# Kernel optimization log

Hardware: AMD Instinct MI355X
Metric: run time of the kernel (lower is better)

## Reference

```python
import jax, jax.numpy as jnp
import numpy as np
import math

B, S, E, H = 8, 1024, 512, 8
EPS = 1e-5

def _ln(x, g, b):
    mu = jnp.mean(x, axis=-1, keepdims=True)
    var = jnp.mean(jnp.square(x - mu), axis=-1, keepdims=True)
    return (x - mu) * jax.lax.rsqrt(var + EPS) * g + b

def setup_inputs() -> dict:
    key = jax.random.key(0)
    ks = iter(jax.random.split(key, 40))
    def w(shape, scale=0.02):
        return jax.random.normal(next(ks), shape, dtype=jnp.float32) * scale
    inp = {
        'x': jax.random.normal(next(ks), (B, S, E), dtype=jnp.float32),
        'cond': jax.random.normal(next(ks), (B, 1, E), dtype=jnp.float32),
        # AdaLN modulation linears (stored as (in,out))
        'g1w': w((E, E)), 'g1b': jnp.zeros((E,), jnp.float32),
        'be1w': w((E, E)), 'be1b': jnp.zeros((E,), jnp.float32),
        'a1w': w((E, E)), 'a1b': jnp.zeros((E,), jnp.float32),
        'g2w': w((E, E)), 'g2b': jnp.zeros((E,), jnp.float32),
        'be2w': w((E, E)), 'be2b': jnp.zeros((E,), jnp.float32),
        'a2w': w((E, E)), 'a2b': jnp.zeros((E,), jnp.float32),
        # LayerNorm affine
        'ln1g': jnp.ones((E,), jnp.float32), 'ln1b': jnp.zeros((E,), jnp.float32),
        'ln2g': jnp.ones((E,), jnp.float32), 'ln2b': jnp.zeros((E,), jnp.float32),
        # attention projections: each head has width E -> out dim H*E
        'wq': w((E, H * E)), 'bq': jnp.zeros((H * E,), jnp.float32),
        'wk': w((E, H * E)), 'bk': jnp.zeros((H * E,), jnp.float32),
        'wv': w((E, H * E)), 'bv': jnp.zeros((H * E,), jnp.float32),
        'lvw': w((H * E, E)), 'lvb': jnp.zeros((E,), jnp.float32),
        # FFN
        'f1w': w((E, 4 * E)), 'f1b': jnp.zeros((4 * E,), jnp.float32),
        'f2w': w((4 * E, E)), 'f2b': jnp.zeros((E,), jnp.float32),
    }
    return inp

def reference(x, cond, g1w, g1b, be1w, be1b, a1w, a1b, g2w, g2b, be2w, be2b, a2w, a2b,
              ln1g, ln1b, ln2g, ln2b, wq, bq, wk, bk, wv, bv, lvw, lvb, f1w, f1b, f2w, f2b):
    # AdaLN modulation signals, each (B,1,E)
    gamma1 = cond @ g1w + g1b
    beta1 = cond @ be1w + be1b
    alpha1 = cond @ a1w + a1b
    gamma2 = cond @ g2w + g2b
    beta2 = cond @ be2w + be2b
    alpha2 = cond @ a2w + a2b

    y = _ln(x, ln1g, ln1b) * (1.0 + gamma1) + beta1
    q = (y @ wq + bq).reshape(B, S, H, E).transpose(0, 2, 1, 3)  # (B,H,S,E)
    k = (y @ wk + bk).reshape(B, S, H, E).transpose(0, 2, 1, 3)
    v = (y @ wv + bv).reshape(B, S, H, E).transpose(0, 2, 1, 3)
    # NOTE: original scales by sqrt(q.size(2)) == sqrt(seq_len), not head_dim
    scale = 1.0 / math.sqrt(S)
    attn = jax.nn.softmax(jnp.einsum('bhse,bhte->bhst', q, k) * scale, axis=-1)
    o = jnp.einsum('bhst,bhte->bhse', attn, v)  # (B,H,S,E)
    o = o.transpose(0, 2, 1, 3).reshape(B, S, H * E)
    y = x + (o @ lvw + lvb) * alpha1

    z = _ln(y, ln2g, ln2b) * (1.0 + gamma2) + beta2
    z = (jax.nn.relu(z @ f1w + f1b) @ f2w + f2b) * alpha2
    return y + z
```

## Files before the change

### kernel.cpp

```cpp
#include <hip/hip_runtime.h>
#include <hip/hip_bf16.h>

typedef __bf16 bf16_t;
typedef bf16_t bf16x8 __attribute__((ext_vector_type(8)));
typedef bf16_t bf16x4 __attribute__((ext_vector_type(4)));
typedef float f32x4 __attribute__((ext_vector_type(4)));

typedef const __attribute__((address_space(1))) void GV;
typedef __attribute__((address_space(3))) void LV;

__device__ __forceinline__ void gload_lds16(const bf16_t* gsrc, bf16_t* ldst) {
    __builtin_amdgcn_global_load_lds((GV*)gsrc, (LV*)ldst, 16, 0, 0);
}

__global__ __launch_bounds__(256) void prep_kernel(
    const float* __restrict__ wq, const float* __restrict__ wk, const float* __restrict__ wv,
    const float* __restrict__ lvw, const float* __restrict__ f1w, const float* __restrict__ f2w,
    bf16_t* __restrict__ wqT, bf16_t* __restrict__ lvwT,
    bf16_t* __restrict__ f1wT, bf16_t* __restrict__ f2wT,
    const float* __restrict__ cond,
    const float* __restrict__ mw0, const float* __restrict__ mw1, const float* __restrict__ mw2,
    const float* __restrict__ mw3, const float* __restrict__ mw4, const float* __restrict__ mw5,
    const float* __restrict__ mc0, const float* __restrict__ mc1, const float* __restrict__ mc2,
    const float* __restrict__ mc3, const float* __restrict__ mc4, const float* __restrict__ mc5,
    float* __restrict__ mod)
{
    __shared__ float sbuf[32 * 33];
    const int bid = blockIdx.x;
    if (bid < 10240) {
        float (*tile)[33] = (float(*)[33])sbuf;
        const float* in; bf16_t* out; int N, nx, K, local;
        if (bid < 6144) {
            const int sec = bid >> 11;
            local = bid & 2047;
            in = (sec == 0) ? wq : ((sec == 1) ? wk : wv);
            out = wqT + (long long)sec * 2097152;
            K = 512; N = 4096; nx = 128;
        } else if (bid < 8192) {
            local = bid - 6144; in = lvw; out = lvwT; K = 4096; N = 512; nx = 16;
        } else if (bid < 9216) {
            local = bid - 8192; in = f1w; out = f1wT; K = 512; N = 2048; nx = 64;
        } else {
            local = bid - 9216; in = f2w; out = f2wT; K = 2048; N = 512; nx = 16;
        }
        const int n0 = (local % nx) * 32, k0 = (local / nx) * 32;
        const int tx = threadIdx.x & 31, ty = threadIdx.x >> 5;
#pragma unroll
        for (int i = 0; i < 32; i += 8)
            tile[ty + i][tx] = in[(long long)(k0 + ty + i) * N + n0 + tx];
        __syncthreads();
#pragma unroll
        for (int i = 0; i < 32; i += 8)
            out[(long long)(n0 + ty + i) * K + k0 + tx] = (bf16_t)tile[tx][ty + i];
    } else {
        float* cs = sbuf;
        const int lb = bid - 10240;
        const int sig = lb >> 3, b = lb & 7;
        const float* w; const float* bi;
        switch (sig) {
            case 0: w = mw0; bi = mc0; break;
            case 1: w = mw1; bi = mc1; break;
            case 2: w = mw2; bi = mc2; break;
            case 3: w = mw3; bi = mc3; break;
            case 4: w = mw4; bi = mc4; break;
            default: w = mw5; bi = mc5; break;
        }
        for (int i = threadIdx.x; i < 512; i += 256) cs[i] = cond[b * 512 + i];
        __syncthreads();
        for (int n = threadIdx.x; n < 512; n += 256) {
            float s0 = 0.f, s1 = 0.f, s2 = 0.f, s3 = 0.f;
            for (int i = 0; i < 512; i += 4) {
                s0 = fmaf(cs[i], w[(long long)i * 512 + n], s0);
                s1 = fmaf(cs[i + 1], w[(long long)(i + 1) * 512 + n], s1);
                s2 = fmaf(cs[i + 2], w[(long long)(i + 2) * 512 + n], s2);
                s3 = fmaf(cs[i + 3], w[(long long)(i + 3) * 512 + n], s3);
            }
            mod[(long long)(sig * 8 + b) * 512 + n] = bi[n] + (s0 + s1) + (s2 + s3);
        }
    }
}

__global__ __launch_bounds__(128) void ln_mod_kernel(
    const float* __restrict__ x, const float* __restrict__ g, const float* __restrict__ be,
    const float* __restrict__ gamma, const float* __restrict__ beta, bf16_t* __restrict__ out)
{
    const int row = blockIdx.x;
    const int b = row >> 10;
    const int t = threadIdx.x;
    const float4 v = reinterpret_cast<const float4*>(x + (long long)row * 512)[t];
    float s = v.x + v.y + v.z + v.w;
    float ss = v.x * v.x + v.y * v.y + v.z * v.z + v.w * v.w;
    for (int o = 32; o; o >>= 1) { s += __shfl_xor(s, o); ss += __shfl_xor(ss, o); }
    __shared__ float red[4];
    if ((t & 63) == 0) { red[t >> 6] = s; red[2 + (t >> 6)] = ss; }
    __syncthreads();
    s = red[0] + red[1]; ss = red[2] + red[3];
    const float mu = s * (1.f / 512.f);
    const float rstd = rsqrtf(ss * (1.f / 512.f) - mu * mu + 1e-5f);
    const float4 gv = reinterpret_cast<const float4*>(g)[t];
    const float4 bv = reinterpret_cast<const float4*>(be)[t];
    const float4 ga = reinterpret_cast<const float4*>(gamma + b * 512)[t];
    const float4 bb = reinterpret_cast<const float4*>(beta + b * 512)[t];
    bf16x4 ov;
    ov[0] = (bf16_t)(((v.x - mu) * rstd * gv.x + bv.x) * (1.f + ga.x) + bb.x);
    ov[1] = (bf16_t)(((v.y - mu) * rstd * gv.y + bv.y) * (1.f + ga.y) + bb.y);
    ov[2] = (bf16_t)(((v.z - mu) * rstd * gv.z + bv.z) * (1.f + ga.z) + bb.z);
    ov[3] = (bf16_t)(((v.w - mu) * rstd * gv.w + bv.w) * (1.f + ga.w) + bb.w);
    reinterpret_cast<bf16x4*>(out + (long long)row * 512)[t] = ov;
}

template <int EPI>
__global__ __launch_bounds__(256) void gemm128_kernel(
    const bf16_t* __restrict__ A, const bf16_t* __restrict__ B,
    const float* __restrict__ bias, void* Cout,
    int M, int N, int K, int lda, int ldb, int ldc)
{
    const int nbx = gridDim.x;
    const int lin = blockIdx.y * nbx + blockIdx.x;
    const int cpx = (nbx * gridDim.y) >> 3;
    const int swz = (lin & 7) * cpx + (lin >> 3);
    const int m0 = (swz / nbx) * 128, n0 = (swz % nbx) * 128;
    const int tid = threadIdx.x, lane = tid & 63, wid = tid >> 6;
    const int wr = wid >> 1, wc = wid & 1;

    __shared__ bf16_t As[16384];
    __shared__ bf16_t Bs[16384];

    f32x4 acc[4][4];
#pragma unroll
    for (int m = 0; m < 4; ++m)
#pragma unroll
        for (int n = 0; n < 4; ++n) acc[m][n] = (f32x4){0.f, 0.f, 0.f, 0.f};

    const int r8 = lane >> 3;
    const int lc = (lane & 7) ^ r8;
    long long aOff[4], bOff[4];
#pragma unroll
    for (int i = 0; i < 4; ++i) {
        const int row = i * 32 + wid * 8 + r8;
        aOff[i] = (long long)(m0 + row) * lda + lc * 8;
        bOff[i] = (long long)(n0 + row) * ldb + lc * 8;
    }

    const int frow = lane & 15, lg = lane >> 4;
    const int p0 = lg ^ (frow & 7);

#pragma unroll
    for (int i = 0; i < 4; ++i) gload_lds16(A + aOff[i], As + i * 2048 + wid * 512);
#pragma unroll
    for (int i = 0; i < 4; ++i) gload_lds16(B + bOff[i], Bs + i * 2048 + wid * 512);

    for (int kt = 0; kt < K; kt += 64) {
        const int cur = (kt >> 6) & 1;
        __syncthreads();
        if (kt + 64 < K) {
            const int nxt = (cur ^ 1) * 8192;
#pragma unroll
            for (int i = 0; i < 4; ++i) gload_lds16(A + aOff[i] + kt + 64, As + nxt + i * 2048 + wid * 512);
#pragma unroll
            for (int i = 0; i < 4; ++i) gload_lds16(B + bOff[i] + kt + 64, Bs + nxt + i * 2048 + wid * 512);
        }
        const bf16_t* Ab = As + cur * 8192;
        const bf16_t* Bb = Bs + cur * 8192;
        __builtin_amdgcn_s_setprio(1);
#pragma unroll
        for (int kk = 0; kk < 2; ++kk) {
            const int pc = p0 ^ (kk << 2);
            bf16x8 af[4], bfv[4];
#pragma unroll
            for (int m = 0; m < 4; ++m)
                af[m] = *reinterpret_cast<const bf16x8*>(Ab + (wr * 64 + m * 16 + frow) * 64 + pc * 8);
#pragma unroll
            for (int n = 0; n < 4; ++n)
                bfv[n] = *reinterpret_cast<const bf16x8*>(Bb + (wc * 64 + n * 16 + frow) * 64 + pc * 8);
#pragma unroll
            for (int m = 0; m < 4; ++m)
#pragma unroll
                for (int n = 0; n < 4; ++n)
                    acc[m][n] = __builtin_amdgcn_mfma_f32_16x16x32_bf16(af[m], bfv[n], acc[m][n], 0, 0, 0);
        }
        __builtin_amdgcn_s_setprio(0);
    }

#pragma unroll
    for (int m = 0; m < 4; ++m) {
        const int gm = m0 + wr * 64 + m * 16 + ((lane >> 4) << 2);
#pragma unroll
        for (int n = 0; n < 4; ++n) {
            const int gn = n0 + wc * 64 + n * 16 + (lane & 15);
            const float bb = bias ? bias[gn] : 0.f;
#pragma unroll
            for (int j = 0; j < 4; ++j) {
                const float v = acc[m][n][j] + bb;
                const int gmj = gm + j;
                if (EPI == 0) {
                    ((bf16_t*)Cout)[(long long)gmj * ldc + gn] = (bf16_t)v;
                } else {
                    ((bf16_t*)Cout)[(long long)gmj * ldc + gn] = (bf16_t)fmaxf(v, 0.f);
                }
            }
        }
    }
}

__global__ __launch_bounds__(256) void gemmqkv_kernel(
    const bf16_t* __restrict__ A, const bf16_t* __restrict__ B,
    const float* __restrict__ bq, const float* __restrict__ bk, const float* __restrict__ bv,
    bf16_t* __restrict__ qkv, bf16_t* __restrict__ vtb)
{
    const int lin = blockIdx.y * 96 + blockIdx.x;
    const int swz = (lin & 7) * 768 + (lin >> 3);
    const int m0 = (swz / 96) * 128, n0 = (swz % 96) * 128;
    const int sec = n0 >> 12;
    const float* bias = (sec == 0) ? bq : ((sec == 1) ? bk : bv);
    const int tid = threadIdx.x, lane = tid & 63, wid = tid >> 6;
    const int wr = wid >> 1, wc = wid & 1;

    __shared__ bf16_t As[16384];
    __shared__ bf16_t Bs[16384];

    f32x4 acc[4][4];
#pragma unroll
    for (int m = 0; m < 4; ++m)
#pragma unroll
        for (int n = 0; n < 4; ++n) acc[m][n] = (f32x4){0.f, 0.f, 0.f, 0.f};

    const int r8 = lane >> 3;
    const int lc = (lane & 7) ^ r8;
    long long aOff[4], bOff[4];
#pragma unroll
    for (int i = 0; i < 4; ++i) {
        const int row = i * 32 + wid * 8 + r8;
        aOff[i] = (long long)(m0 + row) * 512 + lc * 8;
        bOff[i] = (long long)(n0 + row) * 512 + lc * 8;
    }

    const int frow = lane & 15, lg = lane >> 4;
    const int p0 = lg ^ (frow & 7);

#pragma unroll
    for (int i = 0; i < 4; ++i) gload_lds16(A + aOff[i], As + i * 2048 + wid * 512);
#pragma unroll
    for (int i = 0; i < 4; ++i) gload_lds16(B + bOff[i], Bs + i * 2048 + wid * 512);

    for (int kt = 0; kt < 512; kt += 64) {
        const int cur = (kt >> 6) & 1;
        __syncthreads();
        if (kt + 64 < 512) {
            const int nxt = (cur ^ 1) * 8192;
#pragma unroll
            for (int i = 0; i < 4; ++i) gload_lds16(A + aOff[i] + kt + 64, As + nxt + i * 2048 + wid * 512);
#pragma unroll
            for (int i = 0; i < 4; ++i) gload_lds16(B + bOff[i] + kt + 64, Bs + nxt + i * 2048 + wid * 512);
        }
        const bf16_t* Ab = As + cur * 8192;
        const bf16_t* Bb = Bs + cur * 8192;
        __builtin_amdgcn_s_setprio(1);
#pragma unroll
        for (int kk = 0; kk < 2; ++kk) {
            const int pc = p0 ^ (kk << 2);
            bf16x8 af[4], bfv[4];
#pragma unroll
            for (int m = 0; m < 4; ++m)
                af[m] = *reinterpret_cast<const bf16x8*>(Ab + (wr * 64 + m * 16 + frow) * 64 + pc * 8);
#pragma unroll
            for (int n = 0; n < 4; ++n)
                bfv[n] = *reinterpret_cast<const bf16x8*>(Bb + (wc * 64 + n * 16 + frow) * 64 + pc * 8);
#pragma unroll
            for (int m = 0; m < 4; ++m)
#pragma unroll
                for (int n = 0; n < 4; ++n)
                    acc[m][n] = __builtin_amdgcn_mfma_f32_16x16x32_bf16(af[m], bfv[n], acc[m][n], 0, 0, 0);
        }
        __builtin_amdgcn_s_setprio(0);
    }

#pragma unroll
    for (int m = 0; m < 4; ++m) {
        const int gm = m0 + wr * 64 + m * 16 + ((lane >> 4) << 2);
#pragma unroll
        for (int n = 0; n < 4; ++n) {
            const int gn = n0 + wc * 64 + n * 16 + (lane & 15);
            const int gnl = gn & 4095;
            const float bb = bias[gnl];
#pragma unroll
            for (int j = 0; j < 4; ++j) {
                const float v = acc[m][n][j] + bb;
                const int gmj = gm + j;
                if (sec < 2) {
                    qkv[(long long)sec * 33554432 + (long long)gmj * 4096 + gnl] = (bf16_t)v;
                } else {
                    const long long ci =
                        (long long)(((gmj >> 10) * 8 + (gnl >> 9)) * 512 + (gnl & 511)) * 1024 + (gmj & 1023);
                    vtb[ci] = (bf16_t)v;
                }
            }
        }
    }
}

__global__ __launch_bounds__(256) void gemm64_kernel(
    const bf16_t* __restrict__ A, const bf16_t* __restrict__ B,
    const float* __restrict__ bias, float* __restrict__ Cout,
    const float* __restrict__ resid, const float* __restrict__ alpha,
    int M, int N, int K, int lda, int ldb)
{
    const int nbx = gridDim.x;
    const int lin = blockIdx.y * nbx + blockIdx.x;
    const int cpx = (nbx * gridDim.y) >> 3;
    const int swz = (lin & 7) * cpx + (lin >> 3);
    const int m0 = (swz / nbx) * 64, n0 = (swz % nbx) * 128;
    const int tid = threadIdx.x, lane = tid & 63, wid = tid >> 6;
    const int wr = wid >> 1, wc = wid & 1;

    __shared__ bf16_t As[8192];
    __shared__ bf16_t Bs[16384];

    f32x4 acc[2][4];
#pragma unroll
    for (int m = 0; m < 2; ++m)
#pragma unroll
        for (int n = 0; n < 4; ++n) acc[m][n] = (f32x4){0.f, 0.f, 0.f, 0.f};

    const int r8 = lane >> 3;
    const int lc = (lane & 7) ^ r8;
    long long aOff[2], bOff[4];
#pragma unroll
    for (int i = 0; i < 2; ++i)
        aOff[i] = (long long)(m0 + i * 32 + wid * 8 + r8) * lda + lc * 8;
#pragma unroll
    for (int i = 0; i < 4; ++i)
        bOff[i] = (long long)(n0 + i * 32 + wid * 8 + r8) * ldb + lc * 8;

    const int frow = lane & 15, lg = lane >> 4;
    const int p0 = lg ^ (frow & 7);

#pragma unroll
    for (int i = 0; i < 2; ++i) gload_lds16(A + aOff[i], As + i * 2048 + wid * 512);
#pragma unroll
    for (int i = 0; i < 4; ++i) gload_lds16(B + bOff[i], Bs + i * 2048 + wid * 512);

    for (int kt = 0; kt < K; kt += 64) {
        const int cur = (kt >> 6) & 1;
        __syncthreads();
        if (kt + 64 < K) {
#pragma unroll
            for (int i = 0; i < 2; ++i)
                gload_lds16(A + aOff[i] + kt + 64, As + (cur ^ 1) * 4096 + i * 2048 + wid * 512);
#pragma unroll
            for (int i = 0; i < 4; ++i)
                gload_lds16(B + bOff[i] + kt + 64, Bs + (cur ^ 1) * 8192 + i * 2048 + wid * 512);
        }
        const bf16_t* Ab = As + cur * 4096;
        const bf16_t* Bb = Bs + cur * 8192;
        __builtin_amdgcn_s_setprio(1);
#pragma unroll
        for (int kk = 0; kk < 2; ++kk) {
            const int pc = p0 ^ (kk << 2);
            bf16x8 af[2], bfv[4];
#pragma unroll
            for (int m = 0; m < 2; ++m)
                af[m] = *reinterpret_cast<const bf16x8*>(Ab + (wr * 32 + m * 16 + frow) * 64 + pc * 8);
#pragma unroll
            for (int n = 0; n < 4; ++n)
                bfv[n] = *reinterpret_cast<const bf16x8*>(Bb + (wc * 64 + n * 16 + frow) * 64 + pc * 8);
#pragma unroll
            for (int m = 0; m < 2; ++m)
#pragma unroll
                for (int n = 0; n < 4; ++n)
                    acc[m][n] = __builtin_amdgcn_mfma_f32_16x16x32_bf16(af[m], bfv[n], acc[m][n], 0, 0, 0);
        }
        __builtin_amdgcn_s_setprio(0);
    }

#pragma unroll
    for (int m = 0; m < 2; ++m) {
        const int gm = m0 + wr * 32 + m * 16 + ((lane >> 4) << 2);
#pragma unroll
        for (int n = 0; n < 4; ++n) {
            const int gn = n0 + wc * 64 + n * 16 + (lane & 15);
            const float bb = bias[gn];
#pragma unroll
            for (int j = 0; j < 4; ++j) {
                const int gmj = gm + j;
                const long long ci = (long long)gmj * 512 + gn;
                Cout[ci] = resid[ci] + (acc[m][n][j] + bb) * alpha[(gmj >> 10) * 512 + gn];
            }
        }
    }
}

#define FA_LDS 69632
#define SCL 0.04508422132207354f
__global__ __launch_bounds__(256, 2) void flash_kernel(
    bf16_t* __restrict__ qb, const bf16_t* __restrict__ kb, const bf16_t* __restrict__ vtb)
{
    extern __shared__ char smem[];
    bf16_t* Ks = (bf16_t*)smem;
    bf16_t* Vs = (bf16_t*)(smem + 32768);
    char* PB = smem + 65536;
    float* pmaxB = (float*)(smem + 67584);
    float* psumB = (float*)(smem + 68608);

    const int bid = blockIdx.x;
    const int xcd = bid & 7, idx = bid >> 3;
    const int qt = idx & 31, bhl = idx >> 5;
    const int bh = xcd * 8 + bhl;
    const int b = bh >> 3, h = bh & 7;
    const int q0 = qt * 32;
    const int tid = threadIdx.x, lane = tid & 63, wid = tid >> 6;
    const int laneq = lane & 15, lx = lane & 7, lg = lane >> 4;
    const int wk = wid >> 1, wq = wid & 1;
    const int we = wid;

#pragma unroll
    for (int r = 0; r < 8; ++r) {
        const int row = r * 4 + wid;
        gload_lds16(kb + ((long long)(b * 1024 + row) * 8 + h) * 512 + ((lane ^ (row & 7)) << 3),
                    Ks + row * 512);
    }
    const int qi = wq * 16 + laneq;
    bf16x8 qfrag[16];
    {
        const bf16_t* qrow = qb + ((long long)(b * 1024 + q0 + qi) * 8 + h) * 512 + lg * 8;
#pragma unroll
        for (int ks = 0; ks < 16; ++ks) qfrag[ks] = *reinterpret_cast<const bf16x8*>(qrow + ks * 32);
    }
    f32x4 accA[8], accB[8];
#pragma unroll
    for (int e = 0; e < 8; ++e) { accA[e] = (f32x4){0.f,0.f,0.f,0.f}; accB[e] = (f32x4){0.f,0.f,0.f,0.f}; }
    float mS = 0.f, mPA = 0.f, mPB = 0.f, lA = 0.f, lB = 0.f;
    const int rA = wk * 16 + laneq;
    const int qA = laneq, qB = laneq + 16;
    __syncthreads();

    for (int t = 0; t < 32; ++t) {
#pragma unroll
        for (int r = 0; r < 8; ++r) {
            const int e0 = (r * 4 + wid) * 16;
            const int e = e0 + (lane >> 2);
            gload_lds16(vtb + ((long long)bh * 512 + e) * 1024 + t * 32
                            + (((lane & 3) ^ ((e >> 1) & 3)) << 3),
                        Vs + e0 * 32);
        }
        f32x4 s0 = (f32x4){0.f, 0.f, 0.f, 0.f};
        const char* KsB = (const char*)Ks;
        __builtin_amdgcn_s_setprio(1);
#pragma unroll
        for (int ks = 0; ks < 16; ++ks) {
            const int co = (((ks * 4 + lg) ^ lx) << 4);
            bf16x8 a0 = *(const bf16x8*)(KsB + rA * 1024 + co);
            s0 = __builtin_amdgcn_mfma_f32_16x16x32_bf16(a0, qfrag[ks], s0, 0, 0, 0);
        }
        __builtin_amdgcn_s_setprio(0);
        float f[4], pe[4];
#pragma unroll
        for (int j = 0; j < 4; ++j) f[j] = s0[j] * SCL;
        float mloc = fmaxf(fmaxf(f[0], f[1]), fmaxf(f[2], f[3]));
        mloc = fmaxf(mloc, __shfl_xor(mloc, 16));
        mloc = fmaxf(mloc, __shfl_xor(mloc, 32));
        float sl = 0.f;
#pragma unroll
        for (int j = 0; j < 4; ++j) { pe[j] = exp2f(f[j] - mS); sl += pe[j]; }
        sl += __shfl_xor(sl, 16);
        sl += __shfl_xor(sl, 32);
        if (lane < 16) {
            const int si = (t & 1) * 64 + (wq * 16 + lane) * 2 + wk;
            pmaxB[si] = mloc;
            psumB[si] = sl;
        }
        {
            bf16x4 p;
#pragma unroll
            for (int j = 0; j < 4; ++j) p[j] = (bf16_t)pe[j];
            const int g = wk * 4 + lg;
            *(bf16x4*)(PB + qi * 64 + ((((g >> 1) ^ ((qi >> 1) & 3))) << 4) + ((g & 1) << 3)) = p;
        }
        __syncthreads();

        if (t < 31) {
#pragma unroll
            for (int r = 0; r < 8; ++r) {
                const int row = r * 4 + wid;
                gload_lds16(kb + ((long long)(b * 1024 + t * 32 + 32 + row) * 8 + h) * 512
                                + ((lane ^ (row & 7)) << 3),
                            Ks + row * 512);
            }
        }
        const char* VB = (const char*)Vs;
        bf16x8 pA = *(const bf16x8*)(PB + qA * 64 + ((lg ^ ((qA >> 1) & 3)) << 4));
        bf16x8 pBv = *(const bf16x8*)(PB + qB * 64 + ((lg ^ ((qB >> 1) & 3)) << 4));
        __builtin_amdgcn_s_setprio(1);
#pragma unroll
        for (int ef = 0; ef < 8; ++ef) {
            const int re = we * 128 + ef * 16 + laneq;
            bf16x8 av = *(const bf16x8*)(VB + re * 64 + ((lg ^ ((re >> 1) & 3)) << 4));
            accA[ef] = __builtin_amdgcn_mfma_f32_16x16x32_bf16(av, pA, accA[ef], 0, 0, 0);
            accB[ef] = __builtin_amdgcn_mfma_f32_16x16x32_bf16(av, pBv, accB[ef], 0, 0, 0);
        }
        __builtin_amdgcn_s_setprio(0);
        {
            const float* pmax_t = pmaxB + (t & 1) * 64;
            const float* psum_t = psumB + (t & 1) * 64;
            const float2 pmA = *(const float2*)&pmax_t[qA * 2];
            const float2 pmB = *(const float2*)&pmax_t[qB * 2];
            const float2 psA = *(const float2*)&psum_t[qA * 2];
            const float2 psB = *(const float2*)&psum_t[qB * 2];
            mS = fmaxf(mS, wq ? fmaxf(pmB.x, pmB.y) : fmaxf(pmA.x, pmA.y));
            lA += psA.x + psA.y;
            lB += psB.x + psB.y;
            const float mnA = fmaxf(mPA, fmaxf(pmA.x, pmA.y));
            const float mnB = fmaxf(mPB, fmaxf(pmB.x, pmB.y));
            if (__ballot((mnA > mPA) || (mnB > mPB))) {
                const float rsA = exp2f(mPA - mnA), rsB = exp2f(mPB - mnB);
                lA *= rsA; lB *= rsB;
#pragma unroll
                for (int e = 0; e < 8; ++e) {
#pragma unroll
                    for (int j = 0; j < 4; ++j) { accA[e][j] *= rsA; accB[e][j] *= rsB; }
                }
            }
            mPA = mnA; mPB = mnB;
        }
        __syncthreads();
    }

    const float iA = 1.f / lA, iB = 1.f / lB;
#pragma unroll
    for (int ef = 0; ef < 8; ++ef) {
        const int e0 = we * 128 + ef * 16 + lg * 4;
        bf16x4 oA, oB;
#pragma unroll
        for (int j = 0; j < 4; ++j) { oA[j] = (bf16_t)(accA[ef][j] * iA); oB[j] = (bf16_t)(accB[ef][j] * iB); }
        *(bf16x4*)(qb + ((long long)(b * 1024 + q0 + qA) * 8 + h) * 512 + e0) = oA;
        *(bf16x4*)(qb + ((long long)(b * 1024 + q0 + qB) * 8 + h) * 512 + e0) = oB;
    }
}

extern "C" void kernel_launch(void* const* d_in, const int* in_sizes, int n_in,
                              void* d_out, int out_size, void* d_ws, size_t ws_size,
                              hipStream_t stream)
{
    const float* x    = (const float*)d_in[0];
    const float* cond = (const float*)d_in[1];
    const float* g1w  = (const float*)d_in[2];  const float* g1b  = (const float*)d_in[3];
    const float* be1w = (const float*)d_in[4];  const float* be1b = (const float*)d_in[5];
    const float* a1w  = (const float*)d_in[6];  const float* a1b  = (const float*)d_in[7];
    const float* g2w  = (const float*)d_in[8];  const float* g2b  = (const float*)d_in[9];
    const float* be2w = (const float*)d_in[10]; const float* be2b = (const float*)d_in[11];
    const float* a2w  = (const float*)d_in[12]; const float* a2b  = (const float*)d_in[13];
    const float* ln1g = (const float*)d_in[14]; const float* ln1b = (const float*)d_in[15];
    const float* ln2g = (const float*)d_in[16]; const float* ln2b = (const float*)d_in[17];
    const float* wq   = (const float*)d_in[18]; const float* bq   = (const float*)d_in[19];
    const float* wk   = (const float*)d_in[20]; const float* bk   = (const float*)d_in[21];
    const float* wv   = (const float*)d_in[22]; const float* bv   = (const float*)d_in[23];
    const float* lvw  = (const float*)d_in[24]; const float* lvb  = (const float*)d_in[25];
    const float* f1w  = (const float*)d_in[26]; const float* f1b  = (const float*)d_in[27];
    const float* f2w  = (const float*)d_in[28]; const float* f2b  = (const float*)d_in[29];
    (void)in_sizes; (void)n_in; (void)out_size; (void)ws_size;

    char* w8 = (char*)d_ws;
    float*  mod  = (float*)(w8);
    bf16_t* wqT  = (bf16_t*)(w8 + 98304);
    bf16_t* lvwT = (bf16_t*)(w8 + 98304 + 3 * 4194304);
    bf16_t* f1wT = (bf16_t*)(w8 + 98304 + 4 * 4194304);
    bf16_t* f2wT = (bf16_t*)(w8 + 98304 + 4 * 4194304 + 2097152);
    bf16_t* ybf  = (bf16_t*)(w8 + 98304 + 4 * 4194304 + 2 * 2097152);
    bf16_t* qb   = (bf16_t*)(w8 + 98304 + 4 * 4194304 + 2 * 2097152 + 8388608);
    bf16_t* kb   = qb + 33554432;
    bf16_t* vtb  = kb + 33554432;

    (void)hipFuncSetAttribute((const void*)flash_kernel,
                              hipFuncAttributeMaxDynamicSharedMemorySize, FA_LDS);

    const dim3 blk(256);
    prep_kernel<<<10288, blk, 0, stream>>>(wq, wk, wv, lvw, f1w, f2w,
                                           wqT, lvwT, f1wT, f2wT,
                                           cond, g1w, be1w, a1w, g2w, be2w, a2w,
                                           g1b, be1b, a1b, g2b, be2b, a2b, mod);
    ln_mod_kernel<<<8192, 128, 0, stream>>>(x, ln1g, ln1b, mod, mod + 4096, ybf);
    gemmqkv_kernel<<<dim3(96, 64), blk, 0, stream>>>(ybf, wqT, bq, bk, bv, qb, vtb);
    flash_kernel<<<2048, 256, FA_LDS, stream>>>(qb, kb, vtb);
    gemm64_kernel<<<dim3(4, 128), blk, 0, stream>>>(qb, lvwT, lvb, (float*)d_out, x, mod + 8192,
        8192, 512, 4096, 4096, 4096);
    ln_mod_kernel<<<8192, 128, 0, stream>>>((const float*)d_out, ln2g, ln2b,
                                            mod + 12288, mod + 16384, ybf);
    gemm128_kernel<1><<<dim3(16, 64), blk, 0, stream>>>(ybf, f1wT, f1b, qb,
        8192, 2048, 512, 512, 512, 2048);
    gemm64_kernel<<<dim3(4, 128), blk, 0, stream>>>(qb, f2wT, f2b, (float*)d_out,
        (const float*)d_out, mod + 20480,
        8192, 512, 2048, 2048, 2048);
}
```

Baseline: 673.9 us.

## Enlarge QKV GEMM tile to 256x128, drop double buffering, split flash QK accumulators

The QKV projection GEMM now uses 256x128 block tiles, so each wave computes a 128x64 output with 8x4 MFMA accumulators. The grid is halved to match, and B-operand reuse per block goes up. The LDS double-buffered prefetch is replaced by a single buffer that loads and then syncs twice per k-step, which removes the overlap of loads with compute. In the flash kernel, the QK^T dot product now rotates across four independent accumulators to break the serial MFMA dependency chain, summing them at the end at the cost of extra registers.

```diff
diff --git a/kernel.cpp b/kernel.cpp
--- a/kernel.cpp
+++ b/kernel.cpp
@@ -209,75 +209,64 @@
     bf16_t* __restrict__ qkv, bf16_t* __restrict__ vtb)
 {
     const int lin = blockIdx.y * 96 + blockIdx.x;
-    const int swz = (lin & 7) * 768 + (lin >> 3);
-    const int m0 = (swz / 96) * 128, n0 = (swz % 96) * 128;
+    const int swz = (lin & 7) * 384 + (lin >> 3);
+    const int m0 = (swz / 96) * 256, n0 = (swz % 96) * 128;
     const int sec = n0 >> 12;
     const float* bias = (sec == 0) ? bq : ((sec == 1) ? bk : bv);
     const int tid = threadIdx.x, lane = tid & 63, wid = tid >> 6;
     const int wr = wid >> 1, wc = wid & 1;
 
     __shared__ bf16_t As[16384];
-    __shared__ bf16_t Bs[16384];
-
-    f32x4 acc[4][4];
-#pragma unroll
-    for (int m = 0; m < 4; ++m)
+    __shared__ bf16_t Bs[8192];
+
+    f32x4 acc[8][4];
+#pragma unroll
+    for (int m = 0; m < 8; ++m)
 #pragma unroll
         for (int n = 0; n < 4; ++n) acc[m][n] = (f32x4){0.f, 0.f, 0.f, 0.f};
 
     const int r8 = lane >> 3;
     const int lc = (lane & 7) ^ r8;
-    long long aOff[4], bOff[4];
-#pragma unroll
-    for (int i = 0; i < 4; ++i) {
-        const int row = i * 32 + wid * 8 + r8;
-        aOff[i] = (long long)(m0 + row) * 512 + lc * 8;
-        bOff[i] = (long long)(n0 + row) * 512 + lc * 8;
-    }
+    long long aOff[8], bOff[4];
+#pragma unroll
+    for (int i = 0; i < 8; ++i)
+        aOff[i] = (long long)(m0 + i * 32 + wid * 8 + r8) * 512 + lc * 8;
+#pragma unroll
+    for (int i = 0; i < 4; ++i)
+        bOff[i] = (long long)(n0 + i * 32 + wid * 8 + r8) * 512 + lc * 8;
 
     const int frow = lane & 15, lg = lane >> 4;
     const int p0 = lg ^ (frow & 7);
 
-#pragma unroll
-    for (int i = 0; i < 4; ++i) gload_lds16(A + aOff[i], As + i * 2048 + wid * 512);
-#pragma unroll
-    for (int i = 0; i < 4; ++i) gload_lds16(B + bOff[i], Bs + i * 2048 + wid * 512);
-
     for (int kt = 0; kt < 512; kt += 64) {
-        const int cur = (kt >> 6) & 1;
-        __syncthreads();
-        if (kt + 64 < 512) {
-            const int nxt = (cur ^ 1) * 8192;
-#pragma unroll
-            for (int i = 0; i < 4; ++i) gload_lds16(A + aOff[i] + kt + 64, As + nxt + i * 2048 + wid * 512);
-#pragma unroll
-            for (int i = 0; i < 4; ++i) gload_lds16(B + bOff[i] + kt + 64, Bs + nxt + i * 2048 + wid * 512);
-        }
-        const bf16_t* Ab = As + cur * 8192;
-        const bf16_t* Bb = Bs + cur * 8192;
+#pragma unroll
+        for (int i = 0; i < 8; ++i) gload_lds16(A + aOff[i] + kt, As + i * 2048 + wid * 512);
+#pragma unroll
+        for (int i = 0; i < 4; ++i) gload_lds16(B + bOff[i] + kt, Bs + i * 2048 + wid * 512);
+        __syncthreads();
         __builtin_amdgcn_s_setprio(1);
 #pragma unroll
         for (int kk = 0; kk < 2; ++kk) {
             const int pc = p0 ^ (kk << 2);
-            bf16x8 af[4], bfv[4];
-#pragma unroll
-            for (int m = 0; m < 4; ++m)
-                af[m] = *reinterpret_cast<const bf16x8*>(Ab + (wr * 64 + m * 16 + frow) * 64 + pc * 8);
+            bf16x8 bfv[4];
 #pragma unroll
             for (int n = 0; n < 4; ++n)
-                bfv[n] = *reinterpret_cast<const bf16x8*>(Bb + (wc * 64 + n * 16 + frow) * 64 + pc * 8);
-#pragma unroll
-            for (int m = 0; m < 4; ++m)
+                bfv[n] = *reinterpret_cast<const bf16x8*>(Bs + (wc * 64 + n * 16 + frow) * 64 + pc * 8);
+#pragma unroll
+            for (int m = 0; m < 8; ++m) {
+                const bf16x8 af = *reinterpret_cast<const bf16x8*>(As + (wr * 128 + m * 16 + frow) * 64 + pc * 8);
 #pragma unroll
                 for (int n = 0; n < 4; ++n)
-                    acc[m][n] = __builtin_amdgcn_mfma_f32_16x16x32_bf16(af[m], bfv[n], acc[m][n], 0, 0, 0);
+                    acc[m][n] = __builtin_amdgcn_mfma_f32_16x16x32_bf16(af, bfv[n], acc[m][n], 0, 0, 0);
+            }
         }
         __builtin_amdgcn_s_setprio(0);
-    }
-
-#pragma unroll
-    for (int m = 0; m < 4; ++m) {
-        const int gm = m0 + wr * 64 + m * 16 + ((lane >> 4) << 2);
+        __syncthreads();
+    }
+
+#pragma unroll
+    for (int m = 0; m < 8; ++m) {
+        const int gm = m0 + wr * 128 + m * 16 + ((lane >> 4) << 2);
 #pragma unroll
         for (int n = 0; n < 4; ++n) {
             const int gn = n0 + wc * 64 + n * 16 + (lane & 15);
@@ -443,16 +432,19 @@
                             + (((lane & 3) ^ ((e >> 1) & 3)) << 3),
                         Vs + e0 * 32);
         }
-        f32x4 s0 = (f32x4){0.f, 0.f, 0.f, 0.f};
+        f32x4 sacc[4];
+#pragma unroll
+        for (int c = 0; c < 4; ++c) sacc[c] = (f32x4){0.f, 0.f, 0.f, 0.f};
         const char* KsB = (const char*)Ks;
         __builtin_amdgcn_s_setprio(1);
 #pragma unroll
         for (int ks = 0; ks < 16; ++ks) {
             const int co = (((ks * 4 + lg) ^ lx) << 4);
             bf16x8 a0 = *(const bf16x8*)(KsB + rA * 1024 + co);
-            s0 = __builtin_amdgcn_mfma_f32_16x16x32_bf16(a0, qfrag[ks], s0, 0, 0, 0);
+            sacc[ks & 3] = __builtin_amdgcn_mfma_f32_16x16x32_bf16(a0, qfrag[ks], sacc[ks & 3], 0, 0, 0);
         }
         __builtin_amdgcn_s_setprio(0);
+        const f32x4 s0 = (sacc[0] + sacc[1]) + (sacc[2] + sacc[3]);
         float f[4], pe[4];
 #pragma unroll
         for (int j = 0; j < 4; ++j) f[j] = s0[j] * SCL;
@@ -579,7 +571,7 @@
                                            cond, g1w, be1w, a1w, g2w, be2w, a2w,
                                            g1b, be1b, a1b, g2b, be2b, a2b, mod);
     ln_mod_kernel<<<8192, 128, 0, stream>>>(x, ln1g, ln1b, mod, mod + 4096, ybf);
-    gemmqkv_kernel<<<dim3(96, 64), blk, 0, stream>>>(ybf, wqT, bq, bk, bv, qb, vtb);
+    gemmqkv_kernel<<<dim3(96, 32), blk, 0, stream>>>(ybf, wqT, bq, bk, bv, qb, vtb);
     flash_kernel<<<2048, 256, FA_LDS, stream>>>(qb, kb, vtb);
     gemm64_kernel<<<dim3(4, 128), blk, 0, stream>>>(qb, lvwT, lvb, (float*)d_out, x, mod + 8192,
         8192, 512, 4096, 4096, 4096);
```

After: 733.1 us. 8.8% more time.
